# Performance work log

Measured on AMD Instinct MI355X. Metric: run time of the kernel, lower is better.

## Reference

```python
import jax, jax.numpy as jnp
import numpy as np

B, S, NI = 8, 1024, 1024      # batch, seq_len, n_inputs
L, H, P = 128, 128, 64        # n_latents, hidden=n_inputs//8, prototype_dim
EPS_PROTO = 1e-4              # self.epsilon
BN_EPS = 1e-5                 # torch BatchNorm1d default eps


def setup_inputs() -> dict:
    key = jax.random.key(0)
    ks = jax.random.split(key, 4)
    return {
        "x": jax.random.normal(ks[0], (B, S, NI), jnp.float32),
        "W1": jax.random.normal(ks[1], (L, H, NI), jnp.float32) * 0.02,
        "b1": jnp.zeros((L, H), jnp.float32),
        "gamma": jnp.ones((L, H), jnp.float32),
        "beta": jnp.zeros((L, H), jnp.float32),
        "run_mean": jnp.zeros((L, H), jnp.float32),
        "run_var": jnp.ones((L, H), jnp.float32),
        "W2": jax.random.normal(ks[2], (L, P, H), jnp.float32) * 0.02,
        "b2": jnp.zeros((L, P), jnp.float32),
        "prototypes": jax.random.normal(ks[3], (L, P), jnp.float32) * 0.02,
    }


def reference(x, W1, b1, gamma, beta, run_mean, run_var, W2, b2, prototypes):
    Bb, Ss, _ = x.shape
    xf = x.reshape(Bb * Ss, NI)                       # [T, NI]
    # grouped first Linear over all latents at once: [T, L, H]
    h = jnp.einsum('ti,lhi->tlh', xf, W1) + b1
    # Dropout is identity in eval; BatchNorm1d in eval mode (running stats)
    h = (h - run_mean) * jax.lax.rsqrt(run_var + BN_EPS) * gamma + beta
    h = jax.nn.relu(h)
    # grouped second Linear: [T, L, P]
    enc = jnp.einsum('tlh,lph->tlp', h, W2) + b2
    # prototype L2-distance activation
    l2s = jnp.sum((enc - prototypes) ** 2, axis=-1)   # [T, L]
    raw = jnp.log((l2s + 1.0) / (l2s + EPS_PROTO))
    act = raw / jnp.log(1.0 / EPS_PROTO) * 300.0 - 100.0
    return act.reshape(Bb, Ss, L)
```

## Files before the change

kernel.cpp:

```cpp
#include <hip/hip_runtime.h>


#define NTOK 8192
#define NI   1024
#define NL   128
#define NH   128
#define NP   64

typedef __bf16 bf16x8 __attribute__((ext_vector_type(8)));
typedef float f32x4 __attribute__((ext_vector_type(4)));
typedef int   i32x4 __attribute__((ext_vector_type(4)));

static __device__ __forceinline__ unsigned short f2bf(float f) {
  union { float f; unsigned int u; } v; v.f = f;
  const unsigned int u = v.u;
  return (unsigned short)((u + 0x7fffu + ((u >> 16) & 1u)) >> 16);
}

__global__ void cvt_f32_bf16(const float* __restrict__ in,
                             unsigned short* __restrict__ out, int n8) {
  const int i = blockIdx.x * blockDim.x + threadIdx.x;
  if (i >= n8) return;
  const float4* p = (const float4*)in;
  const float4 a = p[2 * i], b = p[2 * i + 1];
  unsigned short v[8] __attribute__((aligned(16))) = {
      f2bf(a.x), f2bf(a.y), f2bf(a.z), f2bf(a.w),
      f2bf(b.x), f2bf(b.y), f2bf(b.z), f2bf(b.w)};
  ((uint4*)out)[i] = *(const uint4*)v;
}

__global__ void quant_rows_i8(const float* __restrict__ in,
                              signed char* __restrict__ outq,
                              float* __restrict__ scale, int nrows) {
  const int row = blockIdx.x * 4 + (threadIdx.x >> 6);
  if (row >= nrows) return;
  const int lane = threadIdx.x & 63;
  const float4* src = (const float4*)(in + (size_t)row * 1024);
  float4 v[4];
  float m = 0.f;
#pragma unroll
  for (int j = 0; j < 4; ++j) {
    v[j] = src[lane + 64 * j];
    m = fmaxf(m, fmaxf(fmaxf(fabsf(v[j].x), fabsf(v[j].y)),
                       fmaxf(fabsf(v[j].z), fabsf(v[j].w))));
  }
#pragma unroll
  for (int s = 1; s < 64; s <<= 1) m = fmaxf(m, __shfl_xor(m, s));
  m = fmaxf(m, 1e-20f);
  const float inv = 127.0f / m;
  if (lane == 0) scale[row] = m * (1.0f / 127.0f);
  unsigned int* dst = (unsigned int*)(outq + (size_t)row * 1024);
#pragma unroll
  for (int j = 0; j < 4; ++j) {
    const float qa = fminf(127.f, fmaxf(-127.f, v[j].x * inv));
    const float qb = fminf(127.f, fmaxf(-127.f, v[j].y * inv));
    const float qc = fminf(127.f, fmaxf(-127.f, v[j].z * inv));
    const float qd = fminf(127.f, fmaxf(-127.f, v[j].w * inv));
    const int a = (int)rintf(qa), b = (int)rintf(qb),
              c = (int)rintf(qc), d = (int)rintf(qd);
    dst[lane + 64 * j] = (unsigned)(a & 255) | ((unsigned)(b & 255) << 8) |
                         ((unsigned)(c & 255) << 16) | ((unsigned)(d & 255) << 24);
  }
}

static __device__ __forceinline__ void async16(const void* g, void* l) {
  __builtin_amdgcn_global_load_lds(
      (const __attribute__((address_space(1))) unsigned int*)g,
      (__attribute__((address_space(3))) unsigned int*)l, 16, 0, 0);
}

__global__ __launch_bounds__(256, 3) void proto_fused(
    const signed char* __restrict__ xq,
    const signed char* __restrict__ w1q,
    const unsigned short* __restrict__ w2b,
    const float* __restrict__ sx,
    const float* __restrict__ sw,
    const float* __restrict__ b1,
    const float* __restrict__ gamma, const float* __restrict__ beta,
    const float* __restrict__ rmean, const float* __restrict__ rvar,
    const float* __restrict__ b2,
    const float* __restrict__ protos,
    float* __restrict__ out)
{
  __shared__ __attribute__((aligned(128))) char smem[49152];
  const int tid  = threadIdx.x;
  const int wave = tid >> 6;
  const int lane = tid & 63;
  const int l15  = lane & 15;
  const int l4   = lane >> 4;
  const int wr   = wave >> 1;
  const int wc   = wave & 1;
  const int t0   = blockIdx.x * 128;
  const int lat  = blockIdx.y;

  const int srow  = lane >> 3;
  const int scolb = ((lane & 7) ^ srow) * 16;

  i32x4 acc[4][4] = {};

#pragma unroll
  for (int i = 0; i < 4; ++i) {
    const int r = wave * 4 + i * 16 + (lane >> 4);
    const int c = (lane & 15) ^ (r & 15);
    async16(w2b + (size_t)lat * NP * NH + r * NH + c * 8,
            smem + 32768 + (wave * 64 + i * 256) * 16);
  }

  auto stage = [&](int ks) {
    const int k0 = ks * 128;
#pragma unroll
    for (int j = 0; j < 4; ++j) {
      const int row = wave * 32 + j * 8 + srow;
      async16(xq + (size_t)(t0 + row) * NI + k0 + scolb,
              smem + (wave * 4 + j) * 1024);
      async16(w1q + (size_t)(lat * NH + row) * NI + k0 + scolb,
              smem + 16384 + (wave * 4 + j) * 1024);
    }
  };

  stage(0);
  const int rx = l15 & 7;
  for (int ks = 0; ks < 8; ++ks) {
    __syncthreads();
#pragma unroll
    for (int kk = 0; kk < 2; ++kk) {
      i32x4 a[4], b[4];
#pragma unroll
      for (int m = 0; m < 4; ++m)
        a[m] = *(const i32x4*)(smem + (wr * 64 + m * 16 + l15) * 128 +
                               (((kk * 4 + l4) ^ rx) << 4));
#pragma unroll
      for (int n = 0; n < 4; ++n)
        b[n] = *(const i32x4*)(smem + 16384 + (wc * 64 + n * 16 + l15) * 128 +
                               (((kk * 4 + l4) ^ rx) << 4));
#pragma unroll
      for (int m = 0; m < 4; ++m)
#pragma unroll
        for (int n = 0; n < 4; ++n)
          acc[m][n] = __builtin_amdgcn_mfma_i32_16x16x64_i8(a[m], b[n], acc[m][n], 0, 0, 0);
    }
    __syncthreads();
    if (ks + 1 < 8) stage(ks + 1);
  }

  float sxv[4][4];
#pragma unroll
  for (int m = 0; m < 4; ++m)
#pragma unroll
    for (int r = 0; r < 4; ++r)
      sxv[m][r] = sx[t0 + wr * 64 + m * 16 + l4 * 4 + r];

#pragma unroll
  for (int n = 0; n < 4; ++n) {
    const int hc = wc * 64 + n * 16 + l15;
    const int gi = lat * NH + hc;
    const float swc = sw[gi];
    const float sc  = gamma[gi] * rsqrtf(rvar[gi] + 1e-5f);
    const float bi  = beta[gi] - rmean[gi] * sc;
    const float bb  = b1[gi];
#pragma unroll
    for (int m = 0; m < 4; ++m)
#pragma unroll
      for (int r = 0; r < 4; ++r) {
        const float hv = (float)acc[m][n][r] * sxv[m][r] * swc;
        float v = (hv + bb) * sc + bi;
        v = v > 0.f ? v : 0.f;
        const int row = wr * 64 + m * 16 + l4 * 4 + r;
        const int pbyte = row * 256 + (((hc >> 3) ^ (row & 15)) << 4) + (hc & 7) * 2;
        *(unsigned short*)(smem + pbyte) = f2bf(v);
      }
  }
  __syncthreads();

  f32x4 acc2[2][4] = {};
#pragma unroll
  for (int kk = 0; kk < 4; ++kk) {
    const int pcsel = kk * 4 + l4;
    bf16x8 a2[2], bw[4];
#pragma unroll
    for (int m = 0; m < 2; ++m) {
      const int row = wave * 32 + m * 16 + l15;
      a2[m] = *(const bf16x8*)(smem + row * 256 + ((pcsel ^ (row & 15)) << 4));
    }
#pragma unroll
    for (int n = 0; n < 4; ++n) {
      const int rp = n * 16 + l15;
      bw[n] = *(const bf16x8*)(smem + 32768 + rp * 256 + ((pcsel ^ (rp & 15)) << 4));
    }
#pragma unroll
    for (int m = 0; m < 2; ++m)
#pragma unroll
      for (int n = 0; n < 4; ++n)
        acc2[m][n] = __builtin_amdgcn_mfma_f32_16x16x32_bf16(a2[m], bw[n], acc2[m][n], 0, 0, 0);
  }

  float pb[4], pp[4];
#pragma unroll
  for (int n = 0; n < 4; ++n) {
    const int p = n * 16 + l15;
    pb[n] = b2[lat * NP + p];
    pp[n] = protos[lat * NP + p];
  }
  const float act_scale = 300.0f / logf(10000.0f);
#pragma unroll
  for (int m = 0; m < 2; ++m)
#pragma unroll
    for (int r = 0; r < 4; ++r) {
      float s = 0.f;
#pragma unroll
      for (int n = 0; n < 4; ++n) {
        const float e = acc2[m][n][r] + pb[n] - pp[n];
        s += e * e;
      }
      s += __shfl_xor(s, 1);
      s += __shfl_xor(s, 2);
      s += __shfl_xor(s, 4);
      s += __shfl_xor(s, 8);
      if (l15 == 0) {
        const float a = logf((s + 1.0f) / (s + 1e-4f)) * act_scale - 100.0f;
        const int trow = wave * 32 + m * 16 + l4 * 4 + r;
        out[(size_t)(t0 + trow) * NL + lat] = a;
      }
    }
}

extern "C" void kernel_launch(void* const* d_in, const int* in_sizes, int n_in,
                              void* d_out, int out_size, void* d_ws, size_t ws_size,
                              hipStream_t stream) {
  const float* x      = (const float*)d_in[0];
  const float* W1     = (const float*)d_in[1];
  const float* b1     = (const float*)d_in[2];
  const float* gamma  = (const float*)d_in[3];
  const float* beta   = (const float*)d_in[4];
  const float* rmean  = (const float*)d_in[5];
  const float* rvar   = (const float*)d_in[6];
  const float* W2     = (const float*)d_in[7];
  const float* b2     = (const float*)d_in[8];
  const float* protos = (const float*)d_in[9];
  float* out = (float*)d_out;

  char* ws = (char*)d_ws;
  signed char*    xq  = (signed char*)ws;
  signed char*    w1q = (signed char*)(ws + (size_t)8 * 1024 * 1024);
  unsigned short* w2b = (unsigned short*)(ws + (size_t)24 * 1024 * 1024);
  float*          sx  = (float*)(ws + (size_t)26 * 1024 * 1024);
  float*          sw  = (float*)(ws + (size_t)26 * 1024 * 1024 + 64 * 1024);

  quant_rows_i8<<<NTOK / 4, 256, 0, stream>>>(x, xq, sx, NTOK);
  quant_rows_i8<<<NL * NH / 4, 256, 0, stream>>>(W1, w1q, sw, NL * NH);
  {
    const int n8w2 = NL * NP * NH / 8;
    cvt_f32_bf16<<<(n8w2 + 255) / 256, 256, 0, stream>>>(W2, w2b, n8w2);
  }

  dim3 grid(NTOK / 128, NL);
  proto_fused<<<grid, 256, 0, stream>>>(xq, w1q, w2b, sx, sw, b1, gamma, beta,
                                        rmean, rvar, b2, protos, out);
}
```

Before: 229.2 us.

## Process two latents per block with 512 threads, sharing x tile loads

Each block now computes two latents (256 W1 rows) for the same 128-token tile using 8 waves. This halves the number of times the quantized x tile is staged into LDS across the grid. The second GEMM and the prototype epilogue now run serially per latent, with W2 loaded per latent and extra barriers. The two row-quantization launches are merged into one kernel to cut launch overhead, and BN/bias constants are folded into a single FMA. The larger block and the new launch bounds change occupancy and register pressure.

Result: slower. 276.9 us (+20.8%).

```diff
diff --git a/kernel.cpp b/kernel.cpp
--- a/kernel.cpp
+++ b/kernel.cpp
@@ -29,18 +29,33 @@
   ((uint4*)out)[i] = *(const uint4*)v;
 }
 
-__global__ void quant_rows_i8(const float* __restrict__ in,
-                              signed char* __restrict__ outq,
-                              float* __restrict__ scale, int nrows) {
+__global__ void quant_rows_i8_dual(const float* __restrict__ x,
+                                   const float* __restrict__ w1,
+                                   signed char* __restrict__ xq,
+                                   signed char* __restrict__ w1q,
+                                   float* __restrict__ sx,
+                                   float* __restrict__ sw) {
   const int row = blockIdx.x * 4 + (threadIdx.x >> 6);
-  if (row >= nrows) return;
   const int lane = threadIdx.x & 63;
-  const float4* src = (const float4*)(in + (size_t)row * 1024);
+  const float* src;
+  unsigned int* dst;
+  float* sp;
+  if (row < NTOK) {
+    src = x + (size_t)row * 1024;
+    dst = (unsigned int*)(xq + (size_t)row * 1024);
+    sp  = sx + row;
+  } else {
+    const int r = row - NTOK;
+    src = w1 + (size_t)r * 1024;
+    dst = (unsigned int*)(w1q + (size_t)r * 1024);
+    sp  = sw + r;
+  }
+  const float4* s4 = (const float4*)src;
   float4 v[4];
   float m = 0.f;
 #pragma unroll
   for (int j = 0; j < 4; ++j) {
-    v[j] = src[lane + 64 * j];
+    v[j] = s4[lane + 64 * j];
     m = fmaxf(m, fmaxf(fmaxf(fabsf(v[j].x), fabsf(v[j].y)),
                        fmaxf(fabsf(v[j].z), fabsf(v[j].w))));
   }
@@ -48,16 +63,13 @@
   for (int s = 1; s < 64; s <<= 1) m = fmaxf(m, __shfl_xor(m, s));
   m = fmaxf(m, 1e-20f);
   const float inv = 127.0f / m;
-  if (lane == 0) scale[row] = m * (1.0f / 127.0f);
-  unsigned int* dst = (unsigned int*)(outq + (size_t)row * 1024);
+  if (lane == 0) *sp = m * (1.0f / 127.0f);
 #pragma unroll
   for (int j = 0; j < 4; ++j) {
-    const float qa = fminf(127.f, fmaxf(-127.f, v[j].x * inv));
-    const float qb = fminf(127.f, fmaxf(-127.f, v[j].y * inv));
-    const float qc = fminf(127.f, fmaxf(-127.f, v[j].z * inv));
-    const float qd = fminf(127.f, fmaxf(-127.f, v[j].w * inv));
-    const int a = (int)rintf(qa), b = (int)rintf(qb),
-              c = (int)rintf(qc), d = (int)rintf(qd);
+    const int a = (int)rintf(fminf(127.f, fmaxf(-127.f, v[j].x * inv)));
+    const int b = (int)rintf(fminf(127.f, fmaxf(-127.f, v[j].y * inv)));
+    const int c = (int)rintf(fminf(127.f, fmaxf(-127.f, v[j].z * inv)));
+    const int d = (int)rintf(fminf(127.f, fmaxf(-127.f, v[j].w * inv)));
     dst[lane + 64 * j] = (unsigned)(a & 255) | ((unsigned)(b & 255) << 8) |
                          ((unsigned)(c & 255) << 16) | ((unsigned)(d & 255) << 24);
   }
@@ -69,7 +81,7 @@
       (__attribute__((address_space(3))) unsigned int*)l, 16, 0, 0);
 }
 
-__global__ __launch_bounds__(256, 3) void proto_fused(
+__global__ __launch_bounds__(512, 4) void proto_fused(
     const signed char* __restrict__ xq,
     const signed char* __restrict__ w1q,
     const unsigned short* __restrict__ w2b,
@@ -88,51 +100,57 @@
   const int lane = tid & 63;
   const int l15  = lane & 15;
   const int l4   = lane >> 4;
-  const int wr   = wave >> 1;
-  const int wc   = wave & 1;
+  const int wr   = wave >> 2;
+  const int wc   = wave & 3;
   const int t0   = blockIdx.x * 128;
-  const int lat  = blockIdx.y;
-
-  const int srow  = lane >> 3;
-  const int scolb = ((lane & 7) ^ srow) * 16;
+  const int lp   = blockIdx.y;
+
+  const signed char* srcA[2];
+  const signed char* srcB[4];
+  int dstA[2], dstB[4];
+#pragma unroll
+  for (int j = 0; j < 2; ++j) {
+    const int p = j * 512 + tid;
+    const int r = p >> 3;
+    srcA[j] = xq + (size_t)(t0 + r) * NI + ((p & 7) ^ (r & 7)) * 16;
+    dstA[j] = p * 16;
+  }
+#pragma unroll
+  for (int j = 0; j < 4; ++j) {
+    const int p = j * 512 + tid;
+    const int r = p >> 3;
+    srcB[j] = w1q + (size_t)(lp * 256 + r) * NI + ((p & 7) ^ (r & 7)) * 16;
+    dstB[j] = 16384 + p * 16;
+  }
 
   i32x4 acc[4][4] = {};
-
-#pragma unroll
-  for (int i = 0; i < 4; ++i) {
-    const int r = wave * 4 + i * 16 + (lane >> 4);
-    const int c = (lane & 15) ^ (r & 15);
-    async16(w2b + (size_t)lat * NP * NH + r * NH + c * 8,
-            smem + 32768 + (wave * 64 + i * 256) * 16);
-  }
 
   auto stage = [&](int ks) {
     const int k0 = ks * 128;
 #pragma unroll
-    for (int j = 0; j < 4; ++j) {
-      const int row = wave * 32 + j * 8 + srow;
-      async16(xq + (size_t)(t0 + row) * NI + k0 + scolb,
-              smem + (wave * 4 + j) * 1024);
-      async16(w1q + (size_t)(lat * NH + row) * NI + k0 + scolb,
-              smem + 16384 + (wave * 4 + j) * 1024);
-    }
+    for (int j = 0; j < 2; ++j) async16(srcA[j] + k0, smem + dstA[j]);
+#pragma unroll
+    for (int j = 0; j < 4; ++j) async16(srcB[j] + k0, smem + dstB[j]);
   };
 
+  int rbA[4], rbB[4];
+#pragma unroll
+  for (int m = 0; m < 4; ++m) rbA[m] = (wr * 64 + m * 16 + l15) * 128;
+#pragma unroll
+  for (int n = 0; n < 4; ++n) rbB[n] = 16384 + (wc * 64 + n * 16 + l15) * 128;
+  const int rx = l15 & 7;
+
   stage(0);
-  const int rx = l15 & 7;
   for (int ks = 0; ks < 8; ++ks) {
     __syncthreads();
 #pragma unroll
     for (int kk = 0; kk < 2; ++kk) {
+      const int koff = ((kk * 4 + l4) ^ rx) << 4;
       i32x4 a[4], b[4];
 #pragma unroll
-      for (int m = 0; m < 4; ++m)
-        a[m] = *(const i32x4*)(smem + (wr * 64 + m * 16 + l15) * 128 +
-                               (((kk * 4 + l4) ^ rx) << 4));
-#pragma unroll
-      for (int n = 0; n < 4; ++n)
-        b[n] = *(const i32x4*)(smem + 16384 + (wc * 64 + n * 16 + l15) * 128 +
-                               (((kk * 4 + l4) ^ rx) << 4));
+      for (int m = 0; m < 4; ++m) a[m] = *(const i32x4*)(smem + rbA[m] + koff);
+#pragma unroll
+      for (int n = 0; n < 4; ++n) b[n] = *(const i32x4*)(smem + rbB[n] + koff);
 #pragma unroll
       for (int m = 0; m < 4; ++m)
 #pragma unroll
@@ -150,66 +168,80 @@
     for (int r = 0; r < 4; ++r)
       sxv[m][r] = sx[t0 + wr * 64 + m * 16 + l4 * 4 + r];
 
+  const int my_ep = wc >> 1;
+  const int c0    = (wc & 1) * 64;
+  const int lg_w  = lp * 2 + my_ep;
+
+  float Kc[4], Cc[4];
+  int cch[4], cin[4];
 #pragma unroll
   for (int n = 0; n < 4; ++n) {
-    const int hc = wc * 64 + n * 16 + l15;
-    const int gi = lat * NH + hc;
-    const float swc = sw[gi];
-    const float sc  = gamma[gi] * rsqrtf(rvar[gi] + 1e-5f);
-    const float bi  = beta[gi] - rmean[gi] * sc;
-    const float bb  = b1[gi];
-#pragma unroll
-    for (int m = 0; m < 4; ++m)
-#pragma unroll
-      for (int r = 0; r < 4; ++r) {
-        const float hv = (float)acc[m][n][r] * sxv[m][r] * swc;
-        float v = (hv + bb) * sc + bi;
-        v = v > 0.f ? v : 0.f;
-        const int row = wr * 64 + m * 16 + l4 * 4 + r;
-        const int pbyte = row * 256 + (((hc >> 3) ^ (row & 15)) << 4) + (hc & 7) * 2;
-        *(unsigned short*)(smem + pbyte) = f2bf(v);
-      }
-  }
-  __syncthreads();
-
-  f32x4 acc2[2][4] = {};
-#pragma unroll
-  for (int kk = 0; kk < 4; ++kk) {
-    const int pcsel = kk * 4 + l4;
-    bf16x8 a2[2], bw[4];
-#pragma unroll
-    for (int m = 0; m < 2; ++m) {
-      const int row = wave * 32 + m * 16 + l15;
-      a2[m] = *(const bf16x8*)(smem + row * 256 + ((pcsel ^ (row & 15)) << 4));
-    }
+    const int col = c0 + n * 16 + l15;
+    const int gi  = lg_w * NH + col;
+    const float sc_ = gamma[gi] * rsqrtf(rvar[gi] + 1e-5f);
+    Kc[n] = sw[gi] * sc_;
+    Cc[n] = b1[gi] * sc_ + beta[gi] - rmean[gi] * sc_;
+    cch[n] = col >> 3;
+    cin[n] = (col & 7) * 2;
+  }
+
+  const float act_scale = 300.0f / logf(10000.0f);
+
+  for (int ep = 0; ep < 2; ++ep) {
+    const int lg = lp * 2 + ep;
+    if (my_ep == ep) {
+#pragma unroll
+      for (int n = 0; n < 4; ++n) {
+#pragma unroll
+        for (int m = 0; m < 4; ++m)
+#pragma unroll
+          for (int r = 0; r < 4; ++r) {
+            float v = fmaf((float)acc[m][n][r] * sxv[m][r], Kc[n], Cc[n]);
+            v = v > 0.f ? v : 0.f;
+            const int row = wr * 64 + m * 16 + l4 * 4 + r;
+            *(unsigned short*)(smem + row * 256 + ((cch[n] ^ (l4 * 4 + r)) << 4) + cin[n]) =
+                f2bf(v);
+          }
+      }
+    }
+#pragma unroll
+    for (int j = 0; j < 2; ++j) {
+      const int q = j * 512 + tid;
+      const int r = q >> 4;
+      const int c = (q & 15) ^ (r & 15);
+      async16(w2b + (size_t)lg * NP * NH + r * NH + c * 8, smem + 32768 + q * 16);
+    }
+    __syncthreads();
+
+    f32x4 acc2[4] = {};
+    const int row2 = wave * 16 + l15;
+#pragma unroll
+    for (int kk = 0; kk < 4; ++kk) {
+      const int kc = kk * 4 + l4;
+      const bf16x8 a2 = *(const bf16x8*)(smem + row2 * 256 + ((kc ^ l15) << 4));
+      bf16x8 bw[4];
+#pragma unroll
+      for (int n = 0; n < 4; ++n) {
+        const int rp = n * 16 + l15;
+        bw[n] = *(const bf16x8*)(smem + 32768 + rp * 256 + ((kc ^ l15) << 4));
+      }
+#pragma unroll
+      for (int n = 0; n < 4; ++n)
+        acc2[n] = __builtin_amdgcn_mfma_f32_16x16x32_bf16(a2, bw[n], acc2[n], 0, 0, 0);
+    }
+
+    float pb[4], pp[4];
 #pragma unroll
     for (int n = 0; n < 4; ++n) {
-      const int rp = n * 16 + l15;
-      bw[n] = *(const bf16x8*)(smem + 32768 + rp * 256 + ((pcsel ^ (rp & 15)) << 4));
-    }
-#pragma unroll
-    for (int m = 0; m < 2; ++m)
-#pragma unroll
-      for (int n = 0; n < 4; ++n)
-        acc2[m][n] = __builtin_amdgcn_mfma_f32_16x16x32_bf16(a2[m], bw[n], acc2[m][n], 0, 0, 0);
-  }
-
-  float pb[4], pp[4];
-#pragma unroll
-  for (int n = 0; n < 4; ++n) {
-    const int p = n * 16 + l15;
-    pb[n] = b2[lat * NP + p];
-    pp[n] = protos[lat * NP + p];
-  }
-  const float act_scale = 300.0f / logf(10000.0f);
-#pragma unroll
-  for (int m = 0; m < 2; ++m)
+      pb[n] = b2[lg * NP + n * 16 + l15];
+      pp[n] = protos[lg * NP + n * 16 + l15];
+    }
 #pragma unroll
     for (int r = 0; r < 4; ++r) {
       float s = 0.f;
 #pragma unroll
       for (int n = 0; n < 4; ++n) {
-        const float e = acc2[m][n][r] + pb[n] - pp[n];
+        const float e = acc2[n][r] + pb[n] - pp[n];
         s += e * e;
       }
       s += __shfl_xor(s, 1);
@@ -218,10 +250,11 @@
       s += __shfl_xor(s, 8);
       if (l15 == 0) {
         const float a = logf((s + 1.0f) / (s + 1e-4f)) * act_scale - 100.0f;
-        const int trow = wave * 32 + m * 16 + l4 * 4 + r;
-        out[(size_t)(t0 + trow) * NL + lat] = a;
-      }
-    }
+        out[(size_t)(t0 + wave * 16 + l4 * 4 + r) * NL + lg] = a;
+      }
+    }
+    __syncthreads();
+  }
 }
 
 extern "C" void kernel_launch(void* const* d_in, const int* in_sizes, int n_in,
@@ -246,14 +279,13 @@
   float*          sx  = (float*)(ws + (size_t)26 * 1024 * 1024);
   float*          sw  = (float*)(ws + (size_t)26 * 1024 * 1024 + 64 * 1024);
 
-  quant_rows_i8<<<NTOK / 4, 256, 0, stream>>>(x, xq, sx, NTOK);
-  quant_rows_i8<<<NL * NH / 4, 256, 0, stream>>>(W1, w1q, sw, NL * NH);
+  quant_rows_i8_dual<<<(NTOK + NL * NH) / 4, 256, 0, stream>>>(x, W1, xq, w1q, sx, sw);
   {
     const int n8w2 = NL * NP * NH / 8;
     cvt_f32_bf16<<<(n8w2 + 255) / 256, 256, 0, stream>>>(W2, w2b, n8w2);
   }
 
-  dim3 grid(NTOK / 128, NL);
-  proto_fused<<<grid, 256, 0, stream>>>(xq, w1q, w2b, sx, sw, b1, gamma, beta,
+  dim3 grid(NTOK / 128, NL / 2);
+  proto_fused<<<grid, 512, 0, stream>>>(xq, w1q, w2b, sx, sw, b1, gamma, beta,
                                         rmean, rvar, b2, protos, out);
 }
```
